# Performance work log

Measured on AMD Instinct MI355X. Metric: run time of the kernel, lower is better.

## Reference

```python
import jax, jax.numpy as jnp
import numpy as np

DIM = 1024
HEADS = 16
ORDER = 3
B, L = 4, 1024  # note: L must equal DIM due to broadcast in original code


def setup_inputs() -> dict:
    key = jax.random.key(0)
    ks = jax.random.split(key, 10)
    D = DIM
    s = 0.02
    inp = {
        "x": jax.random.normal(ks[0], (B, L, D), dtype=jnp.float32),
        "Wq": jax.random.normal(ks[1], (D, D), dtype=jnp.float32) * s,
        "bq": jnp.zeros((D,), jnp.float32),
        "Wk": jax.random.normal(ks[2], (D, D), dtype=jnp.float32) * s,
        "bk": jnp.zeros((D,), jnp.float32),
        "Wv": jax.random.normal(ks[3], (D, D), dtype=jnp.float32) * s,
        "bv": jnp.zeros((D,), jnp.float32),
        "Wo": jax.random.normal(ks[4], (D, D), dtype=jnp.float32) * s,
        "bo": jnp.zeros((D,), jnp.float32),
        # init per module: zeros field, 0.1 strengths
        "torsion_field": jnp.zeros((ORDER, D), jnp.float32),
        "torsion_strength": jnp.ones((ORDER,), jnp.float32) * 0.1,
    }
    return inp


def reference(x, Wq, bq, Wk, bk, Wv, bv, Wo, bo, torsion_field, torsion_strength):
    Bsz, Ln, D = x.shape
    H = HEADS
    hd = D // H

    def proj(W, b):
        y = jnp.einsum('bld,ed->ble', x, W) + b  # Linear: x @ W.T + b
        return y.reshape(Bsz, Ln, H, hd).transpose(0, 2, 1, 3)  # (B,H,L,hd)

    q = proj(Wq, bq)
    k = proj(Wk, bk)
    v = proj(Wv, bv)

    scores = jnp.einsum('bhld,bhmd->bhlm', q, k) / jnp.sqrt(jnp.float32(hd))

    # torsion bias: sum_i strength_i * sin(arange(L)*(i+1)*pi/L) * sigmoid(field_i)
    # (requires L == D for the elementwise product, as in the original)
    pos = jnp.arange(Ln, dtype=jnp.float32)                       # (L,)
    orders = jnp.arange(1, ORDER + 1, dtype=jnp.float32)          # (O,)
    mods = torsion_strength[:, None] * jnp.sin(pos[None, :] * orders[:, None] * jnp.pi / Ln)  # (O,L)
    phases = jax.nn.sigmoid(torsion_field)                        # (O,D), D==L
    bias = jnp.sum(mods * phases, axis=0)                         # (L,)
    scores = scores + bias[None, None, None, :]

    torsion_energy = jnp.sum(torsion_strength ** 2) / ORDER

    attn = jax.nn.softmax(scores, axis=-1)
    out = jnp.einsum('bhlm,bhmd->bhld', attn, v)
    out = out.transpose(0, 2, 1, 3).reshape(Bsz, Ln, D)
    out = jnp.einsum('bld,ed->ble', out, Wo) + bo
    return out, attn, torsion_energy
```

## Files before the change

### kernel.cpp

```cpp
#include <hip/hip_runtime.h>
#include <hip/hip_bf16.h>

typedef __bf16 bf16x8 __attribute__((ext_vector_type(8)));
typedef __bf16 bf16x4 __attribute__((ext_vector_type(4)));
typedef float f32x4 __attribute__((ext_vector_type(4)));

#define GLDS16(gp, lp) \
    __builtin_amdgcn_global_load_lds((__attribute__((address_space(1))) void*)(gp), \
                                     (__attribute__((address_space(3))) void*)(lp), 16, 0, 0)

static __device__ __forceinline__ void bar_nodrain() {
    __builtin_amdgcn_sched_barrier(0);
    asm volatile("s_waitcnt lgkmcnt(0)" ::: "memory");
    __builtin_amdgcn_s_barrier();
    __builtin_amdgcn_sched_barrier(0);
}

__global__ __launch_bounds__(256) void k_convert(
    const float* __restrict__ x, const float* __restrict__ Wq,
    const float* __restrict__ Wk, const float* __restrict__ Wv,
    const float* __restrict__ Wo,
    __bf16* __restrict__ xb, __bf16* __restrict__ wqb, __bf16* __restrict__ wkb,
    __bf16* __restrict__ wvb, __bf16* __restrict__ wob,
    const float* __restrict__ field, const float* __restrict__ strength,
    float* __restrict__ bias_out, float* __restrict__ energy_out)
{
    if (blockIdx.x == 4096) {
        int t = threadIdx.x;
        #pragma unroll
        for (int m = t; m < 1024; m += 256) {
            float acc = 0.f;
            #pragma unroll
            for (int o = 0; o < 3; ++o) {
                float s  = strength[o];
                float ph = 1.f / (1.f + __expf(-field[o * 1024 + m]));
                float tt = (float)(m * (o + 1)) * 3.14159265358979323846f / 1024.f;
                acc += s * sinf(tt) * ph;
            }
            bias_out[m] = acc;
        }
        if (t == 0) {
            float s0 = strength[0], s1 = strength[1], s2 = strength[2];
            energy_out[0] = (s0 * s0 + s1 * s1 + s2 * s2) * (1.f / 3.f);
        }
        return;
    }
    size_t g = (size_t)blockIdx.x * 256 + threadIdx.x;
    size_t e = g * 8;
    const float* src; __bf16* dst; size_t off;
    if (e < 4194304) { src = x; dst = xb; off = e; }
    else {
        size_t t = e - 4194304;
        int w = (int)(t >> 20); off = t & 1048575;
        src = (w == 0 ? Wq : w == 1 ? Wk : w == 2 ? Wv : Wo);
        dst = (w == 0 ? wqb : w == 1 ? wkb : w == 2 ? wvb : wob);
    }
    float4 a = *(const float4*)(src + off);
    float4 b = *(const float4*)(src + off + 4);
    bf16x8 o;
    o[0] = (__bf16)a.x; o[1] = (__bf16)a.y; o[2] = (__bf16)a.z; o[3] = (__bf16)a.w;
    o[4] = (__bf16)b.x; o[5] = (__bf16)b.y; o[6] = (__bf16)b.z; o[7] = (__bf16)b.w;
    *(bf16x8*)(dst + off) = o;
}

template <int MODE, int BN>
__global__ __launch_bounds__(256) void k_gemm(
    const __bf16* __restrict__ A,
    const __bf16* __restrict__ B0, const __bf16* __restrict__ B1, const __bf16* __restrict__ B2,
    const float* __restrict__ bias0, const float* __restrict__ bias1, const float* __restrict__ bias2,
    __bf16* __restrict__ q_ws, __bf16* __restrict__ k_ws, __bf16* __restrict__ vT_ws,
    float* __restrict__ out)
{
    const int K = 1024;
    constexpr int NB = BN / 32;
    __shared__ __bf16 As[128 * 32];
    __shared__ __bf16 Bs[BN * 32];
    __shared__ __bf16 Cs[MODE == 0 ? 128 * 136 : 4];

    int tid = threadIdx.x;
    int w = tid >> 6, l = tid & 63;
    int l15 = l & 15, quad = l >> 4;
    int m0 = blockIdx.y * 128, n0 = blockIdx.x * BN;
    int z = blockIdx.z;

    const __bf16* Bm = (MODE == 1) ? B0 : (z == 0 ? B0 : (z == 1 ? B1 : B2));
    const float*  bv = (MODE == 1) ? bias0 : (z == 0 ? bias0 : (z == 1 ? bias1 : bias2));

    int srow = w * 16 + (l >> 2);
    int scol = (l & 3) * 8;
    const __bf16* gA = A  + (size_t)(m0 + srow) * K + scol;
    const __bf16* gB = Bm + (size_t)(n0 + srow) * K + scol;
    __bf16* lA = As + w * 512;
    __bf16* lB = Bs + w * 512;

    f32x4 zero = {0.f, 0.f, 0.f, 0.f};
    f32x4 acc[4][NB];
    #pragma unroll
    for (int i = 0; i < 4; ++i)
        #pragma unroll
        for (int j = 0; j < NB; ++j) acc[i][j] = zero;

    int wm = w >> 1, wn = w & 1;

    for (int k0 = 0; k0 < K; k0 += 32) {
        __syncthreads();
        GLDS16(gA + k0,           lA);
        GLDS16(gA + 64 * K + k0,  lA + 2048);
        GLDS16(gB + k0,           lB);
        if (BN == 128) GLDS16(gB + 64 * K + k0,  lB + 2048);
        __builtin_amdgcn_s_waitcnt(0);
        __syncthreads();

        bf16x8 af[4], bfr[NB];
        #pragma unroll
        for (int t = 0; t < 4; ++t)
            af[t] = *(const bf16x8*)&As[(wm * 64 + t * 16 + l15) * 32 + quad * 8];
        #pragma unroll
        for (int t = 0; t < NB; ++t)
            bfr[t] = *(const bf16x8*)&Bs[(wn * (BN / 2) + t * 16 + l15) * 32 + quad * 8];
        #pragma unroll
        for (int i = 0; i < 4; ++i)
            #pragma unroll
            for (int j = 0; j < NB; ++j)
                acc[i][j] = __builtin_amdgcn_mfma_f32_16x16x32_bf16(af[i], bfr[j], acc[i][j], 0, 0, 0);
    }

    if constexpr (MODE == 0) {
        if (z == 2) {
            #pragma unroll
            for (int j = 0; j < NB; ++j) {
                int nl = wn * 64 + j * 16 + l15;
                float badd = bv[n0 + nl];
                #pragma unroll
                for (int i = 0; i < 4; ++i) {
                    int ml = wm * 64 + i * 16 + quad * 4;
                    bf16x4 cv;
                    #pragma unroll
                    for (int r = 0; r < 4; ++r) cv[r] = (__bf16)(acc[i][j][r] + badd);
                    *(bf16x4*)&Cs[nl * 136 + ml] = cv;
                }
            }
            __syncthreads();
            int row = tid >> 1;
            int mh  = (tid & 1) * 64;
            int n = n0 + row, h = n >> 6, d = n & 63;
            int b = m0 >> 10;
            int lpos0 = m0 & 1023;
            __bf16* drow = vT_ws + (((size_t)(b * 16 + h)) * 64 + d) * 1024 + lpos0 + mh;
            #pragma unroll
            for (int s2 = 0; s2 < 8; ++s2)
                *(int4*)&drow[s2 * 8] = *(const int4*)&Cs[row * 136 + mh + s2 * 8];
            return;
        }
    }

    #pragma unroll
    for (int i = 0; i < 4; ++i) {
        int mbase = m0 + wm * 64 + i * 16 + quad * 4;
        #pragma unroll
        for (int j = 0; j < NB; ++j) {
            int n = n0 + wn * (BN / 2) + j * 16 + l15;
            float badd = bv[n];
            #pragma unroll
            for (int r = 0; r < 4; ++r) {
                int m = mbase + r;
                float vres = acc[i][j][r] + badd;
                if (MODE == 1) {
                    out[(size_t)m * 1024 + n] = vres;
                } else {
                    int b = m >> 10, lpos = m & 1023, h = n >> 6, d = n & 63;
                    __bf16* dst = (z == 0 ? q_ws : k_ws);
                    dst[(((size_t)(b * 16 + h)) * 1024 + lpos) * 64 + d] = (__bf16)vres;
                }
            }
        }
    }
}

__global__ __launch_bounds__(256, 2) void k_attn(
    const __bf16* __restrict__ qg, const __bf16* __restrict__ kg, const __bf16* __restrict__ vTg,
    const float* __restrict__ bias, float* __restrict__ attn, __bf16* __restrict__ Og)
{
    __shared__ __bf16 q_s[128 * 72];
    __shared__ __bf16 K_s[64 * 72];
    __shared__ __bf16 Vt_s[64 * 72];
    __shared__ __bf16 P_s[128 * 72];
    __shared__ float bias_s[1024];
    __shared__ float rowsum[128];
    __shared__ float rowinv[128];

    int tid = threadIdx.x, w = tid >> 6, l = tid & 63;
    int l15 = l & 15, quad = l >> 4;
    int wm = w >> 1, wn = w & 1;
    int bh = blockIdx.y;
    int m0 = blockIdx.x * 128;

    {
        const __bf16* src = qg + ((size_t)bh * 1024 + m0) * 64;
        for (int i = tid; i < 1024; i += 256) {
            int r = i >> 3, c = (i & 7) * 8;
            *(int4*)&q_s[r * 72 + c] = *(const int4*)&src[(size_t)r * 64 + c];
        }
    }
    *(float4*)&bias_s[tid * 4] = *(const float4*)&bias[tid * 4];
    if (tid < 128) rowsum[tid] = 0.f;

    int sr = tid >> 3;
    int sc = (tid & 7) * 8;
    const __bf16* kbase = kg  + (size_t)bh * 1024 * 64;
    const __bf16* vbase = vTg + (size_t)bh * 64 * 1024;

    int4 kr0 = *(const int4*)&kbase[(size_t)(sr)      * 64 + sc];
    int4 kr1 = *(const int4*)&kbase[(size_t)(sr + 32) * 64 + sc];
    int4 vr0 = *(const int4*)&vbase[(size_t)(sr)      * 1024 + sc];
    int4 vr1 = *(const int4*)&vbase[(size_t)(sr + 32) * 1024 + sc];

    f32x4 zero = {0.f, 0.f, 0.f, 0.f};
    f32x4 accO[4][2];
    #pragma unroll
    for (int i = 0; i < 4; ++i) { accO[i][0] = zero; accO[i][1] = zero; }
    float rs[4];
    #pragma unroll
    for (int i = 0; i < 4; ++i) rs[i] = 0.f;

    for (int pass = 0; pass < 2; ++pass) {
        for (int ch = 0; ch < 16; ++ch) {
            int n0c = ch * 64;
            bar_nodrain();
            *(int4*)&K_s[sr * 72 + sc]        = kr0;
            *(int4*)&K_s[(sr + 32) * 72 + sc] = kr1;
            if (pass == 0) {
                *(int4*)&Vt_s[sr * 72 + sc]        = vr0;
                *(int4*)&Vt_s[(sr + 32) * 72 + sc] = vr1;
            }
            bar_nodrain();

            if (ch < 15) {
                int nn = n0c + 64;
                kr0 = *(const int4*)&kbase[(size_t)(nn + sr)      * 64 + sc];
                kr1 = *(const int4*)&kbase[(size_t)(nn + sr + 32) * 64 + sc];
                if (pass == 0) {
                    vr0 = *(const int4*)&vbase[(size_t)(sr)      * 1024 + nn + sc];
                    vr1 = *(const int4*)&vbase[(size_t)(sr + 32) * 1024 + nn + sc];
                }
            } else if (pass == 0) {
                kr0 = *(const int4*)&kbase[(size_t)(sr)      * 64 + sc];
                kr1 = *(const int4*)&kbase[(size_t)(sr + 32) * 64 + sc];
            }

            f32x4 accT[2][4];
            #pragma unroll
            for (int j = 0; j < 2; ++j)
                #pragma unroll
                for (int i = 0; i < 4; ++i) accT[j][i] = zero;
            __builtin_amdgcn_s_setprio(1);
            #pragma unroll
            for (int ks2 = 0; ks2 < 2; ++ks2) {
                bf16x8 qf[4], kf[2];
                #pragma unroll
                for (int t2 = 0; t2 < 4; ++t2)
                    qf[t2] = *(const bf16x8*)&q_s[(wm * 64 + t2 * 16 + l15) * 72 + ks2 * 32 + quad * 8];
                #pragma unroll
                for (int t2 = 0; t2 < 2; ++t2)
                    kf[t2] = *(const bf16x8*)&K_s[(wn * 32 + t2 * 16 + l15) * 72 + ks2 * 32 + quad * 8];
                #pragma unroll
                for (int j = 0; j < 2; ++j)
                    #pragma unroll
                    for (int i = 0; i < 4; ++i)
                        accT[j][i] = __builtin_amdgcn_mfma_f32_16x16x32_bf16(kf[j], qf[i], accT[j][i], 0, 0, 0);
            }
            __builtin_amdgcn_s_setprio(0);

            f32x4 b4[2];
            #pragma unroll
            for (int j = 0; j < 2; ++j)
                b4[j] = *(const f32x4*)&bias_s[n0c + wn * 32 + j * 16 + quad * 4];

            float p[4][2][4];
            #pragma unroll
            for (int i = 0; i < 4; ++i)
                #pragma unroll
                for (int j = 0; j < 2; ++j)
                    #pragma unroll
                    for (int r = 0; r < 4; ++r)
                        p[i][j][r] = __expf(0.125f * accT[j][i][r] + b4[j][r]);

            if (pass == 0) {
                #pragma unroll
                for (int i = 0; i < 4; ++i)
                    #pragma unroll
                    for (int j = 0; j < 2; ++j)
                        #pragma unroll
                        for (int r = 0; r < 4; ++r)
                            rs[i] += p[i][j][r];
                #pragma unroll
                for (int i = 0; i < 4; ++i)
                    #pragma unroll
                    for (int j = 0; j < 2; ++j) {
                        bf16x4 pv;
                        #pragma unroll
                        for (int r = 0; r < 4; ++r) pv[r] = (__bf16)p[i][j][r];
                        *(bf16x4*)&P_s[(wm * 64 + i * 16 + l15) * 72 + wn * 32 + j * 16 + quad * 4] = pv;
                    }
                bar_nodrain();
                __builtin_amdgcn_s_setprio(1);
                #pragma unroll
                for (int ks2 = 0; ks2 < 2; ++ks2) {
                    bf16x8 af[4], bfr[2];
                    #pragma unroll
                    for (int t2 = 0; t2 < 4; ++t2)
                        af[t2] = *(const bf16x8*)&P_s[(wm * 64 + t2 * 16 + l15) * 72 + ks2 * 32 + quad * 8];
                    #pragma unroll
                    for (int t2 = 0; t2 < 2; ++t2)
                        bfr[t2] = *(const bf16x8*)&Vt_s[(wn * 32 + t2 * 16 + l15) * 72 + ks2 * 32 + quad * 8];
                    #pragma unroll
                    for (int i = 0; i < 4; ++i)
                        #pragma unroll
                        for (int j = 0; j < 2; ++j)
                            accO[i][j] = __builtin_amdgcn_mfma_f32_16x16x32_bf16(af[i], bfr[j], accO[i][j], 0, 0, 0);
                }
                __builtin_amdgcn_s_setprio(0);
            } else {
                float* dst = attn + ((size_t)bh << 20) + (size_t)m0 * 1024;
                #pragma unroll
                for (int i = 0; i < 4; ++i) {
                    int q = wm * 64 + i * 16 + l15;
                    float inv = rowinv[q];
                    #pragma unroll
                    for (int j = 0; j < 2; ++j) {
                        float4 v;
                        v.x = p[i][j][0] * inv; v.y = p[i][j][1] * inv;
                        v.z = p[i][j][2] * inv; v.w = p[i][j][3] * inv;
                        *(float4*)&dst[(size_t)q * 1024 + n0c + wn * 32 + j * 16 + quad * 4] = v;
                    }
                }
            }
        }
        if (pass == 0) {
            #pragma unroll
            for (int i = 0; i < 4; ++i) {
                float s = rs[i];
                s += __shfl_xor(s, 16);
                s += __shfl_xor(s, 32);
                if (quad == 0) atomicAdd(&rowsum[wm * 64 + i * 16 + l15], s);
            }
            bar_nodrain();
            if (tid < 128) rowinv[tid] = 1.f / rowsum[tid];
            bar_nodrain();
            int b = bh >> 4, h = bh & 15;
            #pragma unroll
            for (int i = 0; i < 4; ++i)
                #pragma unroll
                for (int r = 0; r < 4; ++r) {
                    int row = wm * 64 + i * 16 + quad * 4 + r;
                    float inv = rowinv[row];
                    #pragma unroll
                    for (int j = 0; j < 2; ++j) {
                        int d = wn * 32 + j * 16 + l15;
                        Og[((size_t)(b * 1024 + m0 + row)) * 1024 + h * 64 + d] =
                            (__bf16)(accO[i][j][r] * inv);
                    }
                }
        }
    }
}

extern "C" void kernel_launch(void* const* d_in, const int* in_sizes, int n_in,
                              void* d_out, int out_size, void* d_ws, size_t ws_size,
                              hipStream_t stream)
{
    const float* x  = (const float*)d_in[0];
    const float* Wq = (const float*)d_in[1];
    const float* bq = (const float*)d_in[2];
    const float* Wk = (const float*)d_in[3];
    const float* bk = (const float*)d_in[4];
    const float* Wv = (const float*)d_in[5];
    const float* bvv= (const float*)d_in[6];
    const float* Wo = (const float*)d_in[7];
    const float* bo = (const float*)d_in[8];
    const float* tf = (const float*)d_in[9];
    const float* ts = (const float*)d_in[10];

    float* out    = (float*)d_out;
    float* attn   = out + 4194304;
    float* energy = attn + 67108864;

    char* ws = (char*)d_ws;
    float*  bias  = (float*)ws;
    __bf16* xb    = (__bf16*)(ws + 4096);
    __bf16* wqb   = (__bf16*)(ws + 4096 + 8388608);
    __bf16* wkb   = wqb + 1048576;
    __bf16* wvb   = wkb + 1048576;
    __bf16* wob   = wvb + 1048576;
    __bf16* q_ws  = wob + 1048576;
    __bf16* k_ws  = q_ws + 4194304;
    __bf16* vT_ws = k_ws + 4194304;
    __bf16* O_ws  = xb;

    k_convert<<<dim3(4097), dim3(256), 0, stream>>>(x, Wq, Wk, Wv, Wo, xb, wqb, wkb, wvb, wob,
                                                    tf, ts, bias, energy);
    k_gemm<0, 128><<<dim3(8, 32, 3), dim3(256), 0, stream>>>(xb, wqb, wkb, wvb, bq, bk, bvv,
                                                             q_ws, k_ws, vT_ws, nullptr);
    k_attn<<<dim3(8, 64), dim3(256), 0, stream>>>(q_ws, k_ws, vT_ws, bias, attn, O_ws);
    k_gemm<1, 64><<<dim3(16, 32, 1), dim3(256), 0, stream>>>(O_ws, wob, nullptr, nullptr, bo,
                                                             nullptr, nullptr, nullptr, nullptr,
                                                             nullptr, out);
}
```

Baseline: 431.0 us.

## Double-buffer GEMM LDS tiles to overlap global loads with MFMA compute

The projection GEMM main loop now ping-pongs between two LDS buffers for the A and B tiles. The next K-slice is issued with global_load_lds while MFMAs run on the current one, using explicit vmcnt and lgkmcnt waits plus barriers in place of a full drain each step. LDS is merged into one array, and the epilogue staging buffer Cs aliases the tile buffers. This hides global memory latency behind compute, at the cost of more LDS per block and tighter reliance on correct wait and barrier ordering.

```diff
diff --git a/kernel.cpp b/kernel.cpp
--- a/kernel.cpp
+++ b/kernel.cpp
@@ -12,6 +12,13 @@
 static __device__ __forceinline__ void bar_nodrain() {
     __builtin_amdgcn_sched_barrier(0);
     asm volatile("s_waitcnt lgkmcnt(0)" ::: "memory");
+    __builtin_amdgcn_s_barrier();
+    __builtin_amdgcn_sched_barrier(0);
+}
+
+static __device__ __forceinline__ void bar_wait_vm() {
+    __builtin_amdgcn_sched_barrier(0);
+    asm volatile("s_waitcnt vmcnt(0)" ::: "memory");
     __builtin_amdgcn_s_barrier();
     __builtin_amdgcn_sched_barrier(0);
 }
@@ -73,9 +80,12 @@
 {
     const int K = 1024;
     constexpr int NB = BN / 32;
-    __shared__ __bf16 As[128 * 32];
-    __shared__ __bf16 Bs[BN * 32];
-    __shared__ __bf16 Cs[MODE == 0 ? 128 * 136 : 4];
+    __shared__ __bf16 smem[MODE == 0 ? 17408 : 12288];
+    __bf16* As0 = smem;
+    __bf16* As1 = smem + 4096;
+    __bf16* Bs0 = smem + 8192;
+    __bf16* Bs1 = Bs0 + BN * 32;
+    __bf16* Cs  = smem;
 
     int tid = threadIdx.x;
     int w = tid >> 6, l = tid & 63;
@@ -90,8 +100,6 @@
     int scol = (l & 3) * 8;
     const __bf16* gA = A  + (size_t)(m0 + srow) * K + scol;
     const __bf16* gB = Bm + (size_t)(n0 + srow) * K + scol;
-    __bf16* lA = As + w * 512;
-    __bf16* lB = Bs + w * 512;
 
     f32x4 zero = {0.f, 0.f, 0.f, 0.f};
     f32x4 acc[4][NB];
@@ -102,28 +110,43 @@
 
     int wm = w >> 1, wn = w & 1;
 
-    for (int k0 = 0; k0 < K; k0 += 32) {
-        __syncthreads();
-        GLDS16(gA + k0,           lA);
-        GLDS16(gA + 64 * K + k0,  lA + 2048);
-        GLDS16(gB + k0,           lB);
-        if (BN == 128) GLDS16(gB + 64 * K + k0,  lB + 2048);
-        __builtin_amdgcn_s_waitcnt(0);
-        __syncthreads();
-
-        bf16x8 af[4], bfr[NB];
-        #pragma unroll
-        for (int t = 0; t < 4; ++t)
-            af[t] = *(const bf16x8*)&As[(wm * 64 + t * 16 + l15) * 32 + quad * 8];
-        #pragma unroll
-        for (int t = 0; t < NB; ++t)
-            bfr[t] = *(const bf16x8*)&Bs[(wn * (BN / 2) + t * 16 + l15) * 32 + quad * 8];
-        #pragma unroll
-        for (int i = 0; i < 4; ++i)
-            #pragma unroll
-            for (int j = 0; j < NB; ++j)
-                acc[i][j] = __builtin_amdgcn_mfma_f32_16x16x32_bf16(af[i], bfr[j], acc[i][j], 0, 0, 0);
-    }
+#define STAGE(bufA, bufB, kk)                                                  \
+    do {                                                                       \
+        GLDS16(gA + (kk),          (bufA) + w * 512);                          \
+        GLDS16(gA + 64 * K + (kk), (bufA) + w * 512 + 2048);                   \
+        GLDS16(gB + (kk),          (bufB) + w * 512);                          \
+        if (BN == 128) GLDS16(gB + 64 * K + (kk), (bufB) + w * 512 + 2048);    \
+    } while (0)
+
+#define COMPUTE(bufA, bufB)                                                    \
+    do {                                                                       \
+        bf16x8 af[4], bfr[NB];                                                 \
+        _Pragma("unroll")                                                      \
+        for (int t = 0; t < 4; ++t)                                            \
+            af[t] = *(const bf16x8*)&(bufA)[(wm * 64 + t * 16 + l15) * 32 + quad * 8]; \
+        _Pragma("unroll")                                                      \
+        for (int t = 0; t < NB; ++t)                                           \
+            bfr[t] = *(const bf16x8*)&(bufB)[(wn * (BN / 2) + t * 16 + l15) * 32 + quad * 8]; \
+        _Pragma("unroll")                                                      \
+        for (int i = 0; i < 4; ++i)                                            \
+            _Pragma("unroll")                                                  \
+            for (int j = 0; j < NB; ++j)                                       \
+                acc[i][j] = __builtin_amdgcn_mfma_f32_16x16x32_bf16(af[i], bfr[j], acc[i][j], 0, 0, 0); \
+    } while (0)
+
+    STAGE(As0, Bs0, 0);
+    for (int k0 = 0; k0 < K; k0 += 64) {
+        bar_wait_vm();
+        STAGE(As1, Bs1, k0 + 32);
+        COMPUTE(As0, Bs0);
+        bar_nodrain();
+        bar_wait_vm();
+        if (k0 + 64 < K) STAGE(As0, Bs0, k0 + 64);
+        COMPUTE(As1, Bs1);
+        bar_nodrain();
+    }
+#undef STAGE
+#undef COMPUTE
 
     if constexpr (MODE == 0) {
         if (z == 2) {
```

New measurement: 428.0 us. No clear change (-0.7%).
